# Performance work log

Measured on AMD Instinct MI355X. Metric: run time of the kernel, lower is better.

## Reference

```python
import jax, jax.numpy as jnp
import numpy as np

B, T, N, F_IN = 8, 12, 10000, 1
H = 32          # hidden_size
K = 2           # gnn_kernel (diffusion steps)
HORIZON = 12
E = 320000      # n_nodes * avg_degree 32


def setup_inputs() -> dict:
    key = jax.random.key(0)
    ks = jax.random.split(key, 12)
    s = 0.1  # weight scale to keep GRU in sane range
    return {
        "x": jax.random.normal(ks[0], (B, T, N, F_IN), jnp.float32),
        "edge_index": jax.random.randint(ks[1], (2, E), 0, N, dtype=jnp.int64),
        "edge_weight": jax.random.uniform(ks[2], (E,), jnp.float32),
        "enc_w": jax.random.normal(ks[3], (F_IN, H), jnp.float32) * s,
        "enc_b": jnp.zeros((H,), jnp.float32),
        "node_emb": jax.random.normal(ks[4], (N, H), jnp.float32) * s,
        "w_ih": jax.random.normal(ks[5], (3 * H, H), jnp.float32) * s,
        "w_hh": jax.random.normal(ks[6], (3 * H, H), jnp.float32) * s,
        "b_ih": jnp.zeros((3 * H,), jnp.float32),
        "b_hh": jnp.zeros((3 * H,), jnp.float32),
        "filt_w": jax.random.normal(ks[7], ((2 * K + 1) * H, H), jnp.float32) * s,
        "filt_b": jnp.zeros((H,), jnp.float32),
        "dec_w": jax.random.normal(ks[8], (H, F_IN * HORIZON), jnp.float32) * s,
        "dec_b": jnp.zeros((F_IN * HORIZON,), jnp.float32),
    }


def _gru_last(xs, w_ih, w_hh, b_ih, b_hh):
    # xs: [t, bn, H] -> last hidden state [bn, H]
    t, bn, h = xs.shape
    gx = jnp.einsum('tbh,gh->tbg', xs, w_ih) + b_ih  # [t, bn, 3H]

    def step(hid, gx_t):
        gh = hid @ w_hh.T + b_hh
        xr, xz, xn = jnp.split(gx_t, 3, axis=-1)
        hr, hz, hn = jnp.split(gh, 3, axis=-1)
        r = jax.nn.sigmoid(xr + hr)
        z = jax.nn.sigmoid(xz + hz)
        n_ = jnp.tanh(xn + r * hn)
        hid = (1.0 - z) * n_ + z * hid
        return hid, None

    h0 = jnp.zeros((bn, h), xs.dtype)
    h_last, _ = jax.lax.scan(step, h0, gx)
    return h_last


def _propagate(x, src, tgt, w, n):
    # x: [b, n, H]; out[:, tgt] += w * x[:, src]
    msgs = x[:, src, :] * w[None, :, None]  # [b, E, H]
    return jnp.zeros_like(x).at[:, tgt, :].add(msgs)


def reference(x, edge_index, edge_weight, enc_w, enc_b, node_emb,
              w_ih, w_hh, b_ih, b_hh, filt_w, filt_b, dec_w, dec_b):
    b, t, n, f_in = x.shape
    h = enc_w.shape[1]

    # ---- encoder + node embeddings ----
    x_enc = x @ enc_w + enc_b                       # [b, t, n, H]
    x_emb = x_enc + node_emb[None, None]            # broadcast add

    # ---- temporal GRU (per node, batch_first, last state) ----
    xs = jnp.transpose(x_emb, (1, 0, 2, 3)).reshape(t, b * n, h)
    h_time = _gru_last(xs, w_ih, w_hh, b_ih, b_hh).reshape(b, n, h)

    # ---- DiffConv: k-hop forward + backward diffusion ----
    src, tgt = edge_index[0], edge_index[1]
    deg_f = jnp.zeros((n,), edge_weight.dtype).at[tgt].add(edge_weight)
    w_f = edge_weight / jnp.where(deg_f[tgt] > 0, deg_f[tgt], 1.0)
    deg_b = jnp.zeros((n,), edge_weight.dtype).at[src].add(edge_weight)
    w_b = edge_weight / jnp.where(deg_b[src] > 0, deg_b[src], 1.0)

    outs = [h_time]  # root weight
    x_sup = h_time
    for _ in range(K):  # forward transition hops
        x_sup = _propagate(x_sup, src, tgt, w_f, n)
        outs.append(x_sup)
    x_sup = h_time
    for _ in range(K):  # backward (reversed edges) hops
        x_sup = _propagate(x_sup, tgt, src, w_b, n)
        outs.append(x_sup)
    z = jnp.concatenate(outs, axis=-1) @ filt_w + filt_b  # [b, n, H]

    # ---- decoder + rearrange 'b n (t f) -> b t n f' ----
    out = z @ dec_w + dec_b                                # [b, n, horizon*f_in]
    out = out.reshape(b, n, HORIZON, f_in)
    return jnp.transpose(out, (0, 2, 1, 3))                # [b, horizon, n, f_in]
```

## Files before the change

### kernel.cpp

```cpp
#include <hip/hip_runtime.h>
#include <hip/hip_fp16.h>

#define BB 8
#define TT 12
#define NN 10000
#define HH 32
#define EE 320000
#define HOR 12
#define NCB 157

static __device__ __forceinline__ float sigm(float x) {
    return __builtin_amdgcn_rcpf(1.0f + __expf(-x));
}
static __device__ __forceinline__ float tanh_fast(float x) {
    return 1.0f - 2.0f * __builtin_amdgcn_rcpf(1.0f + __expf(2.0f * x));
}
static __device__ __forceinline__ float2 uph2(unsigned u) {
    __half2 h = *(__half2*)&u;
    return __half22float2(h);
}
static __device__ __forceinline__ unsigned pkh2(float a, float b) {
    __half2 h = __floats2half2_rn(a, b);
    return *(unsigned*)&h;
}

typedef _Float16 f16x4 __attribute__((ext_vector_type(4)));
typedef float    f32x4 __attribute__((ext_vector_type(4)));

__global__ void k_zero(uint4* __restrict__ p, int n4) {
    int i = blockIdx.x * blockDim.x + threadIdx.x;
    if (i < n4) p[i] = (uint4){0u, 0u, 0u, 0u};
}

__global__ void k_cbhist(const float* __restrict__ node_emb, const float* __restrict__ enc_b,
                     const float* __restrict__ w_ih, const float* __restrict__ b_ih,
                     const float* __restrict__ b_hh,
                     const float* __restrict__ enc_w, const float* __restrict__ filt_w,
                     const float* __restrict__ filt_b, const float* __restrict__ dec_w,
                     const float* __restrict__ dec_b,
                     float* __restrict__ CB, float* __restrict__ A,
                     float* __restrict__ W2, float* __restrict__ b2,
                     const int* __restrict__ ei,
                     int* cnt_f, int* cnt_b) {
    __shared__ float sw[96*36];
    __shared__ float semb[64*36];
    __shared__ float sbias[96];
    int bid = blockIdx.x;
    int tid = threadIdx.x;
    if (bid < NCB) {
        int n0 = bid * 64;
        for (int i = tid; i < 96*32; i += 256) {
            int g = i >> 5, h = i & 31;
            sw[g*36 + h] = w_ih[i];
        }
        for (int i = tid; i < 64*32; i += 256) {
            int row = i >> 5, h = i & 31;
            int n = n0 + row; if (n >= NN) n = NN-1;
            semb[row*36 + h] = enc_b[h] + node_emb[(size_t)n*32 + h];
        }
        if (tid < 96) sbias[tid] = b_ih[tid] + (tid < 64 ? b_hh[tid] : 0.f);
        __syncthreads();
        #pragma unroll 1
        for (int i = 0; i < 24; i++) {
            int o = i*256 + tid;
            int row = o / 96, g = o - row*96;
            int n = n0 + row;
            if (n < NN) {
                float s = sbias[g];
                const float4* ev = (const float4*)(semb + row*36);
                const float4* wv = (const float4*)(sw + g*36);
                #pragma unroll
                for (int q = 0; q < 8; q++) {
                    float4 e = ev[q], w = wv[q];
                    s = fmaf(e.x, w.x, s); s = fmaf(e.y, w.y, s);
                    s = fmaf(e.z, w.z, s); s = fmaf(e.w, w.w, s);
                }
                CB[(size_t)n*96 + g] = s;
            }
        }
    } else if (bid == NCB) {
        for (int i = tid; i < 96 + 160*12 + 12; i += blockDim.x) {
            if (i < 96) {
                float s = 0.f;
                for (int h = 0; h < HH; h++) s += enc_w[h] * w_ih[i*HH + h];
                A[i] = s;
            } else if (i < 96 + 1920) {
                int j = i - 96; int c = j / 12, o = j % 12;
                float s = 0.f;
                for (int h = 0; h < HH; h++) s += filt_w[c*HH + h] * dec_w[h*12 + o];
                W2[j] = s;
            } else {
                int o = i - 2016;
                float s = dec_b[o];
                for (int h = 0; h < HH; h++) s += filt_b[h] * dec_w[h*12 + o];
                b2[o] = s;
            }
        }
    } else {
        int e = (bid - NCB - 1) * 256 + tid;
        int s = ei[e], t = ei[EE + e];
        atomicAdd(&cnt_f[t], 1);
        atomicAdd(&cnt_b[s], 1);
    }
}

__global__ void k_scan(const int* __restrict__ cnt_f, int* off_f, int* cur_f,
                       const int* __restrict__ cnt_b, int* off_b, int* cur_b) {
    const int* cnt; int* off; int* cur;
    if (blockIdx.x == 0) { cnt = cnt_f; off = off_f; cur = cur_f; }
    else                 { cnt = cnt_b; off = off_b; cur = cur_b; }
    __shared__ int part[1024];
    int t = threadIdx.x;
    const int CH = (NN + 1023) / 1024;
    int beg = t * CH, end = min(beg + CH, NN);
    int s = 0;
    for (int i = beg; i < end; i++) s += cnt[i];
    part[t] = s;
    __syncthreads();
    for (int d = 1; d < 1024; d <<= 1) {
        int add = (t >= d) ? part[t - d] : 0;
        __syncthreads();
        part[t] += add;
        __syncthreads();
    }
    int run = part[t] - s;
    for (int i = beg; i < end; i++) {
        off[i] = run; cur[i] = run; run += cnt[i];
    }
    if (t == 1023) off[NN] = part[1023];
}

__global__ void k_fill(const int* __restrict__ ei, const float* __restrict__ ew,
                       int* cur_f, int* csr_f_idx, float* csr_f_w,
                       int* cur_b, int* csr_b_idx, float* csr_b_w) {
    int e = blockIdx.x * blockDim.x + threadIdx.x;
    int s = ei[e], t = ei[EE + e]; float w = ew[e];
    int pf = atomicAdd(&cur_f[t], 1); csr_f_idx[pf] = s; csr_f_w[pf] = w;
    int pb = atomicAdd(&cur_b[s], 1); csr_b_idx[pb] = t; csr_b_w[pb] = w;
}

__global__ __launch_bounds__(256) void k_gru(const float* __restrict__ x,
                      const float* __restrict__ CB, const float* __restrict__ Ag,
                      const float* __restrict__ w_hh, const float* __restrict__ b_hh,
                      __half* __restrict__ hout16) {
    __shared__ unsigned sW[1536];
    __shared__ __half  shh[4][16*40];
    __shared__ float   sx[64][12];
    int tid = threadIdx.x;
    int r0b = blockIdx.x * 64;

    for (int d = tid; d < 1536; d += 256) {
        int fi = d >> 1, epair = d & 1;
        int l = fi & 63, tk = fi >> 6;
        int gt = tk >> 1, kh = tk & 1;
        int gate = 16*gt + (l & 15);
        int k = kh*16 + ((l >> 4) << 2) + 2*epair;
        sW[d] = pkh2(w_hh[gate*32 + k], w_hh[gate*32 + k + 1]);
    }
    for (int i = tid; i < 64*12; i += 256) {
        int row = i / 12, t = i - row*12;
        int r = r0b + row; int b = r / NN, n = r - b*NN;
        sx[row][t] = x[((size_t)b*TT + t)*NN + n];
    }
    __syncthreads();

    const int wv = tid >> 6, l = tid & 63;
    const int c = l & 15, m = l >> 4;
    const int r0w = r0b + wv*16;

    int bb[4], nn_[4];
    #pragma unroll
    for (int q = 0; q < 4; q++) {
        int r = r0w + 4*m + q;
        bb[q] = r / NN; nn_[q] = r - bb[q]*NN;
    }

    float cNx[2][4];
    f32x4 crv[2], czv[2], cnv[2];
    float aRj[2], aZj[2], aNj[2], bn0c[2];
    #pragma unroll
    for (int t2 = 0; t2 < 2; t2++) {
        int j = 16*t2 + c;
        #pragma unroll
        for (int q = 0; q < 4; q++) {
            const float* cb = CB + (size_t)nn_[q]*96;
            crv[t2][q] = cb[j];
            czv[t2][q] = cb[32 + j];
            cNx[t2][q] = cb[64 + j];
        }
        bn0c[t2] = b_hh[64 + j];
        cnv[t2] = (f32x4){bn0c[t2], bn0c[t2], bn0c[t2], bn0c[t2]};
        aRj[t2] = Ag[j]; aZj[t2] = Ag[32 + j]; aNj[t2] = Ag[64 + j];
    }

    f16x4 bf[12];
    #pragma unroll
    for (int i = 0; i < 12; i++) {
        unsigned long long v = *(const unsigned long long*)(sW + (i*64 + l)*2);
        bf[i] = __builtin_bit_cast(f16x4, v);
    }

    __half* hb = shh[wv];
    float own[2][4];
    {
        #pragma unroll
        for (int t2 = 0; t2 < 2; t2++)
        #pragma unroll
        for (int q = 0; q < 4; q++) {
            float xv = sx[wv*16 + 4*m + q][0];
            float rr = sigm(fmaf(xv, aRj[t2], crv[t2][q]));
            float zz = sigm(fmaf(xv, aZj[t2], czv[t2][q]));
            float nv = tanh_fast(fmaf(xv, aNj[t2], cNx[t2][q]) + rr * bn0c[t2]);
            own[t2][q] = (1.f - zz) * nv;
        }
    }
    #pragma unroll
    for (int t2 = 0; t2 < 2; t2++)
    #pragma unroll
    for (int q = 0; q < 4; q++)
        hb[(4*m + q)*40 + 16*t2 + c] = __float2half_rn(own[t2][q]);

    #pragma unroll 1
    for (int t = 1; t < TT; t++) {
        asm volatile("s_waitcnt lgkmcnt(0)" ::: "memory");
        __builtin_amdgcn_sched_barrier(0);
        unsigned long long va0 = *(const unsigned long long*)(hb + c*40 + m*4);
        unsigned long long va1 = *(const unsigned long long*)(hb + c*40 + 16 + m*4);
        f16x4 a0 = __builtin_bit_cast(f16x4, va0);
        f16x4 a1 = __builtin_bit_cast(f16x4, va1);
        float xq[4];
        #pragma unroll
        for (int q = 0; q < 4; q++) xq[q] = sx[wv*16 + 4*m + q][t];

        f32x4 aR[2], aZ[2], aN[2];
        #pragma unroll
        for (int t2 = 0; t2 < 2; t2++) {
            aR[t2] = __builtin_amdgcn_mfma_f32_16x16x16f16(a0, bf[(t2    )*2    ], crv[t2], 0, 0, 0);
            aR[t2] = __builtin_amdgcn_mfma_f32_16x16x16f16(a1, bf[(t2    )*2 + 1], aR[t2], 0, 0, 0);
            aZ[t2] = __builtin_amdgcn_mfma_f32_16x16x16f16(a0, bf[(2 + t2)*2    ], czv[t2], 0, 0, 0);
            aZ[t2] = __builtin_amdgcn_mfma_f32_16x16x16f16(a1, bf[(2 + t2)*2 + 1], aZ[t2], 0, 0, 0);
            aN[t2] = __builtin_amdgcn_mfma_f32_16x16x16f16(a0, bf[(4 + t2)*2    ], cnv[t2], 0, 0, 0);
            aN[t2] = __builtin_amdgcn_mfma_f32_16x16x16f16(a1, bf[(4 + t2)*2 + 1], aN[t2], 0, 0, 0);
        }
        #pragma unroll
        for (int t2 = 0; t2 < 2; t2++)
        #pragma unroll
        for (int q = 0; q < 4; q++) {
            float rr = sigm(fmaf(xq[q], aRj[t2], aR[t2][q]));
            float zz = sigm(fmaf(xq[q], aZj[t2], aZ[t2][q]));
            float nv = tanh_fast(fmaf(xq[q], aNj[t2], cNx[t2][q]) + rr * aN[t2][q]);
            own[t2][q] = (1.f - zz) * nv + zz * own[t2][q];
        }
        if (t < TT-1) {
            #pragma unroll
            for (int t2 = 0; t2 < 2; t2++)
            #pragma unroll
            for (int q = 0; q < 4; q++)
                hb[(4*m + q)*40 + 16*t2 + c] = __float2half_rn(own[t2][q]);
        }
    }
    #pragma unroll
    for (int t2 = 0; t2 < 2; t2++)
    #pragma unroll
    for (int q = 0; q < 4; q++)
        hout16[((size_t)nn_[q]*BB + bb[q])*HH + 16*t2 + c] = __float2half(own[t2][q]);
}

__global__ __launch_bounds__(256) void k_prop(
        const __half* __restrict__ xF, const __half* __restrict__ xB,
        __half* __restrict__ yF16, __half* __restrict__ yB16,
        const int* __restrict__ offF, const int* __restrict__ idxF, const float* __restrict__ wF,
        const int* __restrict__ offB, const int* __restrict__ idxB, const float* __restrict__ wB) {
    int wid = threadIdx.x >> 6;
    int l   = threadIdx.x & 63;
    int nd = blockIdx.x * 4 + wid;
    int n = nd >> 1, dir = nd & 1;
    const unsigned* xu = (const unsigned*)(dir ? xB : xF);
    const int* off = dir ? offB : offF;
    const int* idx = dir ? idxB : idxF;
    const float* w = dir ? wB : wF;

    int e0 = off[n], e1 = off[n+1];
    float a0 = 0.f, a1 = 0.f, a2 = 0.f, a3 = 0.f, ws = 0.f;
    int e = e0;
    for (; e + 8 <= e1; e += 8) {
        int   s0 = idx[e],   s1 = idx[e+1], s2 = idx[e+2], s3 = idx[e+3];
        int   s4 = idx[e+4], s5 = idx[e+5], s6 = idx[e+6], s7 = idx[e+7];
        float w0 = w[e],     w1 = w[e+1],   w2 = w[e+2],   w3 = w[e+3];
        float w4 = w[e+4],   w5 = w[e+5],   w6 = w[e+6],   w7 = w[e+7];
        uint2 u0 = *(const uint2*)(xu + ((size_t)s0 << 7) + 2*l);
        uint2 u1 = *(const uint2*)(xu + ((size_t)s1 << 7) + 2*l);
        uint2 u2 = *(const uint2*)(xu + ((size_t)s2 << 7) + 2*l);
        uint2 u3 = *(const uint2*)(xu + ((size_t)s3 << 7) + 2*l);
        uint2 u4 = *(const uint2*)(xu + ((size_t)s4 << 7) + 2*l);
        uint2 u5 = *(const uint2*)(xu + ((size_t)s5 << 7) + 2*l);
        uint2 u6 = *(const uint2*)(xu + ((size_t)s6 << 7) + 2*l);
        uint2 u7 = *(const uint2*)(xu + ((size_t)s7 << 7) + 2*l);
        ws += ((w0 + w1) + (w2 + w3)) + ((w4 + w5) + (w6 + w7));
        float2 f;
        f = uph2(u0.x); a0 = fmaf(w0, f.x, a0); a1 = fmaf(w0, f.y, a1);
        f = uph2(u0.y); a2 = fmaf(w0, f.x, a2); a3 = fmaf(w0, f.y, a3);
        f = uph2(u1.x); a0 = fmaf(w1, f.x, a0); a1 = fmaf(w1, f.y, a1);
        f = uph2(u1.y); a2 = fmaf(w1, f.x, a2); a3 = fmaf(w1, f.y, a3);
        f = uph2(u2.x); a0 = fmaf(w2, f.x, a0); a1 = fmaf(w2, f.y, a1);
        f = uph2(u2.y); a2 = fmaf(w2, f.x, a2); a3 = fmaf(w2, f.y, a3);
        f = uph2(u3.x); a0 = fmaf(w3, f.x, a0); a1 = fmaf(w3, f.y, a1);
        f = uph2(u3.y); a2 = fmaf(w3, f.x, a2); a3 = fmaf(w3, f.y, a3);
        f = uph2(u4.x); a0 = fmaf(w4, f.x, a0); a1 = fmaf(w4, f.y, a1);
        f = uph2(u4.y); a2 = fmaf(w4, f.x, a2); a3 = fmaf(w4, f.y, a3);
        f = uph2(u5.x); a0 = fmaf(w5, f.x, a0); a1 = fmaf(w5, f.y, a1);
        f = uph2(u5.y); a2 = fmaf(w5, f.x, a2); a3 = fmaf(w5, f.y, a3);
        f = uph2(u6.x); a0 = fmaf(w6, f.x, a0); a1 = fmaf(w6, f.y, a1);
        f = uph2(u6.y); a2 = fmaf(w6, f.x, a2); a3 = fmaf(w6, f.y, a3);
        f = uph2(u7.x); a0 = fmaf(w7, f.x, a0); a1 = fmaf(w7, f.y, a1);
        f = uph2(u7.y); a2 = fmaf(w7, f.x, a2); a3 = fmaf(w7, f.y, a3);
    }
    for (; e < e1; ++e) {
        int s0 = idx[e]; float w0 = w[e];
        uint2 u0 = *(const uint2*)(xu + ((size_t)s0 << 7) + 2*l);
        ws += w0;
        float2 f;
        f = uph2(u0.x); a0 = fmaf(w0, f.x, a0); a1 = fmaf(w0, f.y, a1);
        f = uph2(u0.y); a2 = fmaf(w0, f.x, a2); a3 = fmaf(w0, f.y, a3);
    }
    float inv = ws > 0.f ? __builtin_amdgcn_rcpf(ws) : 1.0f;
    a0 *= inv; a1 *= inv; a2 *= inv; a3 *= inv;
    unsigned* yh = (unsigned*)(dir ? yB16 : yF16);
    uint2 oh; oh.x = pkh2(a0, a1); oh.y = pkh2(a2, a3);
    *(uint2*)(yh + ((size_t)n << 7) + 2*l) = oh;
}

__global__ __launch_bounds__(256) void k_dec(const __half* __restrict__ p0,
                     const __half* __restrict__ p1, const __half* __restrict__ p2,
                     const __half* __restrict__ p3, const __half* __restrict__ p4,
                     const float* __restrict__ W2, const float* __restrict__ b2,
                     float* __restrict__ out) {
    __shared__ float sW[1920];
    __shared__ float sb[12];
    __shared__ float part[128][13];
    int tid = threadIdx.x;
    for (int i = tid; i < 1920; i += 256) sW[i] = W2[i];
    if (tid < 12) sb[tid] = b2[tid];
    __syncthreads();
    int lr = tid & 127, half = tid >> 7;
    int r = blockIdx.x * 128 + lr;
    int b = r / NN, n = r - b*NN;
    size_t base = ((size_t)n * BB + b) * HH;
    float a[12];
    if (half == 0) {
        uint4 v[12];
        {
            const uint4* q0 = (const uint4*)(p0 + base);
            const uint4* q1 = (const uint4*)(p1 + base);
            const uint4* q2 = (const uint4*)(p2 + base);
            #pragma unroll
            for (int q = 0; q < 4; q++) { v[q] = q0[q]; v[4+q] = q1[q]; v[8+q] = q2[q]; }
        }
        #pragma unroll
        for (int o = 0; o < 12; o++) a[o] = sb[o];
        #pragma unroll
        for (int pi = 0; pi < 3; pi++)
        #pragma unroll
        for (int q = 0; q < 4; q++) {
            uint4 vv = v[pi*4 + q];
            float2 f0 = uph2(vv.x), f1 = uph2(vv.y), f2 = uph2(vv.z), f3 = uph2(vv.w);
            float pv[8] = {f0.x, f0.y, f1.x, f1.y, f2.x, f2.y, f3.x, f3.y};
            #pragma unroll
            for (int k = 0; k < 8; k++) {
                const float* wrow = sW + (pi*32 + q*8 + k) * 12;
                #pragma unroll
                for (int o = 0; o < 12; o++) a[o] = fmaf(pv[k], wrow[o], a[o]);
            }
        }
    } else {
        uint4 v[8];
        {
            const uint4* q3 = (const uint4*)(p3 + base);
            const uint4* q4 = (const uint4*)(p4 + base);
            #pragma unroll
            for (int q = 0; q < 4; q++) { v[q] = q3[q]; v[4+q] = q4[q]; }
        }
        #pragma unroll
        for (int o = 0; o < 12; o++) a[o] = 0.f;
        #pragma unroll
        for (int pi = 0; pi < 2; pi++)
        #pragma unroll
        for (int q = 0; q < 4; q++) {
            uint4 vv = v[pi*4 + q];
            float2 f0 = uph2(vv.x), f1 = uph2(vv.y), f2 = uph2(vv.z), f3 = uph2(vv.w);
            float pv[8] = {f0.x, f0.y, f1.x, f1.y, f2.x, f2.y, f3.x, f3.y};
            #pragma unroll
            for (int k = 0; k < 8; k++) {
                const float* wrow = sW + ((pi+3)*32 + q*8 + k) * 12;
                #pragma unroll
                for (int o = 0; o < 12; o++) a[o] = fmaf(pv[k], wrow[o], a[o]);
            }
        }
        #pragma unroll
        for (int o = 0; o < 12; o++) part[lr][o] = a[o];
    }
    __syncthreads();
    if (half == 0) {
        #pragma unroll
        for (int t = 0; t < HOR; t++)
            out[((size_t)(b*HOR + t))*NN + n] = a[t] + part[lr][t];
    }
}

extern "C" void kernel_launch(void* const* d_in, const int* in_sizes, int n_in,
                              void* d_out, int out_size, void* d_ws, size_t ws_size,
                              hipStream_t stream) {
    const float* x      = (const float*)d_in[0];
    const int*   ei     = (const int*)d_in[1];
    const float* ew     = (const float*)d_in[2];
    const float* enc_w  = (const float*)d_in[3];
    const float* enc_b  = (const float*)d_in[4];
    const float* nemb   = (const float*)d_in[5];
    const float* w_ih   = (const float*)d_in[6];
    const float* w_hh   = (const float*)d_in[7];
    const float* b_ih   = (const float*)d_in[8];
    const float* b_hh   = (const float*)d_in[9];
    const float* filt_w = (const float*)d_in[10];
    const float* filt_b = (const float*)d_in[11];
    const float* dec_w  = (const float*)d_in[12];
    const float* dec_b  = (const float*)d_in[13];
    float* out = (float*)d_out;

    char* p = (char*)d_ws;
    auto alloc = [&](size_t bytes) -> char* {
        char* q = p; p += (bytes + 255) & ~(size_t)255; return q;
    };
    char* zero_base = p;
    int*   cnt_f = (int*)  alloc((size_t)NN*4);
    int*   cnt_b = (int*)  alloc((size_t)NN*4);
    size_t zero_bytes = (size_t)(p - zero_base);
    int zero_n4 = (int)(zero_bytes / 16);

    const size_t SROW = (size_t)BB*NN*HH;
    __half* h16    = (__half*)alloc(SROW*2);
    __half* a16    = (__half*)alloc(SROW*2);
    __half* b16    = (__half*)alloc(SROW*2);
    __half* c16    = (__half*)alloc(SROW*2);
    __half* d16    = (__half*)alloc(SROW*2);
    float* CB     = (float*)alloc((size_t)NN*96*4);
    float* A      = (float*)alloc(96*4);
    float* W2     = (float*)alloc(1920*4);
    float* b2     = (float*)alloc(12*4);
    int*   off_f  = (int*)  alloc((size_t)(NN+1)*4);
    int*   off_b  = (int*)  alloc((size_t)(NN+1)*4);
    int*   cur_f  = (int*)  alloc((size_t)NN*4);
    int*   cur_b  = (int*)  alloc((size_t)NN*4);
    int*   cfi    = (int*)  alloc((size_t)EE*4);
    float* cfw    = (float*)alloc((size_t)EE*4);
    int*   cbi    = (int*)  alloc((size_t)EE*4);
    float* cbw    = (float*)alloc((size_t)EE*4);

    k_zero<<<(zero_n4 + 255)/256, 256, 0, stream>>>((uint4*)zero_base, zero_n4);

    k_cbhist<<<NCB + 1 + EE/256, 256, 0, stream>>>(nemb, enc_b, w_ih, b_ih, b_hh,
                                       enc_w, filt_w, filt_b, dec_w, dec_b,
                                       CB, A, W2, b2, ei, cnt_f, cnt_b);
    k_scan<<<2, 1024, 0, stream>>>(cnt_f, off_f, cur_f, cnt_b, off_b, cur_b);
    k_fill<<<EE/256, 256, 0, stream>>>(ei, ew, cur_f, cfi, cfw, cur_b, cbi, cbw);

    k_gru<<<1250, 256, 0, stream>>>(x, CB, A, w_hh, b_hh, h16);

    k_prop<<<5000, 256, 0, stream>>>(h16, h16, a16, c16,
                                     off_f, cfi, cfw, off_b, cbi, cbw);
    k_prop<<<5000, 256, 0, stream>>>(a16, c16, b16, d16,
                                     off_f, cfi, cfw, off_b, cbi, cbw);

    k_dec<<<625, 256, 0, stream>>>(h16, a16, b16, c16, d16, W2, b2, out);
}
```

Measured before the change: 222.3 us.

## Fuse CSR fill into GRU launch, interleave edge data, fuse second hop with decoder

The CSR fill kernel is merged into the GRU launch as extra blocks, so edge scattering can overlap with the recurrent compute. Edge index and weight are packed into one uint2 array, so each gather reads a single 8-byte record. The second diffusion hop is fused with the decoder: hop-2 results stay in shared memory and feed the output projection directly, which removes two intermediate fp16 buffers and a separate decoder launch. In exchange, the decoder phase now runs on only 64 of 256 threads per block, and the GRU blocks may lose occupancy from sharing the grid with fill blocks.

```diff
diff --git a/kernel.cpp b/kernel.cpp
--- a/kernel.cpp
+++ b/kernel.cpp
@@ -130,23 +130,27 @@
     if (t == 1023) off[NN] = part[1023];
 }
 
-__global__ void k_fill(const int* __restrict__ ei, const float* __restrict__ ew,
-                       int* cur_f, int* csr_f_idx, float* csr_f_w,
-                       int* cur_b, int* csr_b_idx, float* csr_b_w) {
-    int e = blockIdx.x * blockDim.x + threadIdx.x;
-    int s = ei[e], t = ei[EE + e]; float w = ew[e];
-    int pf = atomicAdd(&cur_f[t], 1); csr_f_idx[pf] = s; csr_f_w[pf] = w;
-    int pb = atomicAdd(&cur_b[s], 1); csr_b_idx[pb] = t; csr_b_w[pb] = w;
-}
-
-__global__ __launch_bounds__(256) void k_gru(const float* __restrict__ x,
+__global__ __launch_bounds__(256) void k_grufill(const float* __restrict__ x,
                       const float* __restrict__ CB, const float* __restrict__ Ag,
                       const float* __restrict__ w_hh, const float* __restrict__ b_hh,
-                      __half* __restrict__ hout16) {
+                      __half* __restrict__ hout16,
+                      const int* __restrict__ ei, const float* __restrict__ ew,
+                      int* cur_f, uint2* __restrict__ cfe,
+                      int* cur_b, uint2* __restrict__ cbe) {
+    int tid = threadIdx.x;
+    if (blockIdx.x >= 1250) {
+        int e = (blockIdx.x - 1250) * 256 + tid;
+        int s = ei[e], t = ei[EE + e]; float w = ew[e];
+        unsigned wb = __float_as_uint(w);
+        int pf = atomicAdd(&cur_f[t], 1);
+        uint2 vf; vf.x = (unsigned)s; vf.y = wb; cfe[pf] = vf;
+        int pb = atomicAdd(&cur_b[s], 1);
+        uint2 vb; vb.x = (unsigned)t; vb.y = wb; cbe[pb] = vb;
+        return;
+    }
     __shared__ unsigned sW[1536];
     __shared__ __half  shh[4][16*40];
     __shared__ float   sx[64][12];
-    int tid = threadIdx.x;
     int r0b = blockIdx.x * 64;
 
     for (int d = tid; d < 1536; d += 256) {
@@ -266,36 +270,27 @@
         hout16[((size_t)nn_[q]*BB + bb[q])*HH + 16*t2 + c] = __float2half(own[t2][q]);
 }
 
-__global__ __launch_bounds__(256) void k_prop(
-        const __half* __restrict__ xF, const __half* __restrict__ xB,
-        __half* __restrict__ yF16, __half* __restrict__ yB16,
-        const int* __restrict__ offF, const int* __restrict__ idxF, const float* __restrict__ wF,
-        const int* __restrict__ offB, const int* __restrict__ idxB, const float* __restrict__ wB) {
-    int wid = threadIdx.x >> 6;
-    int l   = threadIdx.x & 63;
-    int nd = blockIdx.x * 4 + wid;
-    int n = nd >> 1, dir = nd & 1;
-    const unsigned* xu = (const unsigned*)(dir ? xB : xF);
-    const int* off = dir ? offB : offF;
-    const int* idx = dir ? idxB : idxF;
-    const float* w = dir ? wB : wF;
-
-    int e0 = off[n], e1 = off[n+1];
-    float a0 = 0.f, a1 = 0.f, a2 = 0.f, a3 = 0.f, ws = 0.f;
+static __device__ __forceinline__ void gather_node(
+        const unsigned* __restrict__ xu, const uint2* __restrict__ ef,
+        int e0, int e1, int l, float& a0, float& a1, float& a2, float& a3) {
+    float ws = 0.f;
+    a0 = a1 = a2 = a3 = 0.f;
     int e = e0;
     for (; e + 8 <= e1; e += 8) {
-        int   s0 = idx[e],   s1 = idx[e+1], s2 = idx[e+2], s3 = idx[e+3];
-        int   s4 = idx[e+4], s5 = idx[e+5], s6 = idx[e+6], s7 = idx[e+7];
-        float w0 = w[e],     w1 = w[e+1],   w2 = w[e+2],   w3 = w[e+3];
-        float w4 = w[e+4],   w5 = w[e+5],   w6 = w[e+6],   w7 = w[e+7];
-        uint2 u0 = *(const uint2*)(xu + ((size_t)s0 << 7) + 2*l);
-        uint2 u1 = *(const uint2*)(xu + ((size_t)s1 << 7) + 2*l);
-        uint2 u2 = *(const uint2*)(xu + ((size_t)s2 << 7) + 2*l);
-        uint2 u3 = *(const uint2*)(xu + ((size_t)s3 << 7) + 2*l);
-        uint2 u4 = *(const uint2*)(xu + ((size_t)s4 << 7) + 2*l);
-        uint2 u5 = *(const uint2*)(xu + ((size_t)s5 << 7) + 2*l);
-        uint2 u6 = *(const uint2*)(xu + ((size_t)s6 << 7) + 2*l);
-        uint2 u7 = *(const uint2*)(xu + ((size_t)s7 << 7) + 2*l);
+        uint2 q0 = ef[e],   q1 = ef[e+1], q2 = ef[e+2], q3 = ef[e+3];
+        uint2 q4 = ef[e+4], q5 = ef[e+5], q6 = ef[e+6], q7 = ef[e+7];
+        float w0 = __uint_as_float(q0.y), w1 = __uint_as_float(q1.y);
+        float w2 = __uint_as_float(q2.y), w3 = __uint_as_float(q3.y);
+        float w4 = __uint_as_float(q4.y), w5 = __uint_as_float(q5.y);
+        float w6 = __uint_as_float(q6.y), w7 = __uint_as_float(q7.y);
+        uint2 u0 = *(const uint2*)(xu + ((size_t)q0.x << 7) + 2*l);
+        uint2 u1 = *(const uint2*)(xu + ((size_t)q1.x << 7) + 2*l);
+        uint2 u2 = *(const uint2*)(xu + ((size_t)q2.x << 7) + 2*l);
+        uint2 u3 = *(const uint2*)(xu + ((size_t)q3.x << 7) + 2*l);
+        uint2 u4 = *(const uint2*)(xu + ((size_t)q4.x << 7) + 2*l);
+        uint2 u5 = *(const uint2*)(xu + ((size_t)q5.x << 7) + 2*l);
+        uint2 u6 = *(const uint2*)(xu + ((size_t)q6.x << 7) + 2*l);
+        uint2 u7 = *(const uint2*)(xu + ((size_t)q7.x << 7) + 2*l);
         ws += ((w0 + w1) + (w2 + w3)) + ((w4 + w5) + (w6 + w7));
         float2 f;
         f = uph2(u0.x); a0 = fmaf(w0, f.x, a0); a1 = fmaf(w0, f.y, a1);
@@ -316,8 +311,9 @@
         f = uph2(u7.y); a2 = fmaf(w7, f.x, a2); a3 = fmaf(w7, f.y, a3);
     }
     for (; e < e1; ++e) {
-        int s0 = idx[e]; float w0 = w[e];
-        uint2 u0 = *(const uint2*)(xu + ((size_t)s0 << 7) + 2*l);
+        uint2 q0 = ef[e];
+        float w0 = __uint_as_float(q0.y);
+        uint2 u0 = *(const uint2*)(xu + ((size_t)q0.x << 7) + 2*l);
         ws += w0;
         float2 f;
         f = uph2(u0.x); a0 = fmaf(w0, f.x, a0); a1 = fmaf(w0, f.y, a1);
@@ -325,85 +321,103 @@
     }
     float inv = ws > 0.f ? __builtin_amdgcn_rcpf(ws) : 1.0f;
     a0 *= inv; a1 *= inv; a2 *= inv; a3 *= inv;
+}
+
+__global__ __launch_bounds__(256) void k_prop(
+        const __half* __restrict__ xF, const __half* __restrict__ xB,
+        __half* __restrict__ yF16, __half* __restrict__ yB16,
+        const int* __restrict__ offF, const uint2* __restrict__ efF,
+        const int* __restrict__ offB, const uint2* __restrict__ efB) {
+    int wid = threadIdx.x >> 6;
+    int l   = threadIdx.x & 63;
+    int nd = blockIdx.x * 4 + wid;
+    int n = nd >> 1, dir = nd & 1;
+    const unsigned* xu = (const unsigned*)(dir ? xB : xF);
+    const int* off = dir ? offB : offF;
+    const uint2* ef = dir ? efB : efF;
+    float a0, a1, a2, a3;
+    gather_node(xu, ef, off[n], off[n+1], l, a0, a1, a2, a3);
     unsigned* yh = (unsigned*)(dir ? yB16 : yF16);
     uint2 oh; oh.x = pkh2(a0, a1); oh.y = pkh2(a2, a3);
     *(uint2*)(yh + ((size_t)n << 7) + 2*l) = oh;
 }
 
-__global__ __launch_bounds__(256) void k_dec(const __half* __restrict__ p0,
-                     const __half* __restrict__ p1, const __half* __restrict__ p2,
-                     const __half* __restrict__ p3, const __half* __restrict__ p4,
-                     const float* __restrict__ W2, const float* __restrict__ b2,
-                     float* __restrict__ out) {
+__global__ __launch_bounds__(256) void k_prop2dec(
+        const __half* __restrict__ aF, const __half* __restrict__ cBk,
+        const __half* __restrict__ h16,
+        const int* __restrict__ offF, const uint2* __restrict__ efF,
+        const int* __restrict__ offB, const uint2* __restrict__ efB,
+        const float* __restrict__ W2, const float* __restrict__ b2,
+        float* __restrict__ out) {
     __shared__ float sW[1920];
     __shared__ float sb[12];
-    __shared__ float part[128][13];
+    __shared__ unsigned spc[4][2][128];
     int tid = threadIdx.x;
     for (int i = tid; i < 1920; i += 256) sW[i] = W2[i];
     if (tid < 12) sb[tid] = b2[tid];
+    int wv = tid >> 6, l = tid & 63;
+    int n = blockIdx.x * 4 + wv;
+    {
+        float a0, a1, a2, a3;
+        gather_node((const unsigned*)aF, efF, offF[n], offF[n+1], l, a0, a1, a2, a3);
+        spc[wv][0][2*l]   = pkh2(a0, a1);
+        spc[wv][0][2*l+1] = pkh2(a2, a3);
+    }
+    {
+        float a0, a1, a2, a3;
+        gather_node((const unsigned*)cBk, efB, offB[n], offB[n+1], l, a0, a1, a2, a3);
+        spc[wv][1][2*l]   = pkh2(a0, a1);
+        spc[wv][1][2*l+1] = pkh2(a2, a3);
+    }
     __syncthreads();
-    int lr = tid & 127, half = tid >> 7;
-    int r = blockIdx.x * 128 + lr;
-    int b = r / NN, n = r - b*NN;
-    size_t base = ((size_t)n * BB + b) * HH;
-    float a[12];
-    if (half == 0) {
-        uint4 v[12];
-        {
-            const uint4* q0 = (const uint4*)(p0 + base);
-            const uint4* q1 = (const uint4*)(p1 + base);
-            const uint4* q2 = (const uint4*)(p2 + base);
+    if (tid < 64) {
+        int nl = tid >> 4;
+        int b  = (tid >> 1) & 7;
+        int th = tid & 1;
+        int node = blockIdx.x * 4 + nl;
+        size_t base = ((size_t)node * BB + b) * HH;
+        float a[6];
+        #pragma unroll
+        for (int o = 0; o < 6; o++) a[o] = sb[6*th + o];
+        const __half* gp[3] = {h16, aF, cBk};
+        const int wo[3] = {0, 32, 96};
+        #pragma unroll
+        for (int gi = 0; gi < 3; gi++) {
+            const uint4* pp = (const uint4*)(gp[gi] + base);
+            const float* wbase = sW + wo[gi]*12 + 6*th;
             #pragma unroll
-            for (int q = 0; q < 4; q++) { v[q] = q0[q]; v[4+q] = q1[q]; v[8+q] = q2[q]; }
-        }
-        #pragma unroll
-        for (int o = 0; o < 12; o++) a[o] = sb[o];
-        #pragma unroll
-        for (int pi = 0; pi < 3; pi++)
-        #pragma unroll
-        for (int q = 0; q < 4; q++) {
-            uint4 vv = v[pi*4 + q];
-            float2 f0 = uph2(vv.x), f1 = uph2(vv.y), f2 = uph2(vv.z), f3 = uph2(vv.w);
-            float pv[8] = {f0.x, f0.y, f1.x, f1.y, f2.x, f2.y, f3.x, f3.y};
+            for (int q = 0; q < 4; q++) {
+                uint4 v = pp[q];
+                float2 f0 = uph2(v.x), f1 = uph2(v.y), f2 = uph2(v.z), f3 = uph2(v.w);
+                float pv[8] = {f0.x, f0.y, f1.x, f1.y, f2.x, f2.y, f3.x, f3.y};
+                #pragma unroll
+                for (int k = 0; k < 8; k++) {
+                    const float* wrow = wbase + (q*8 + k)*12;
+                    #pragma unroll
+                    for (int o = 0; o < 6; o++) a[o] = fmaf(pv[k], wrow[o], a[o]);
+                }
+            }
+        }
+        #pragma unroll
+        for (int dir = 0; dir < 2; dir++) {
+            const uint4* pp = (const uint4*)&spc[nl][dir][b*16];
+            const float* wbase = sW + (64 + dir*64)*12 + 6*th;
             #pragma unroll
-            for (int k = 0; k < 8; k++) {
-                const float* wrow = sW + (pi*32 + q*8 + k) * 12;
+            for (int q = 0; q < 4; q++) {
+                uint4 v = pp[q];
+                float2 f0 = uph2(v.x), f1 = uph2(v.y), f2 = uph2(v.z), f3 = uph2(v.w);
+                float pv[8] = {f0.x, f0.y, f1.x, f1.y, f2.x, f2.y, f3.x, f3.y};
                 #pragma unroll
-                for (int o = 0; o < 12; o++) a[o] = fmaf(pv[k], wrow[o], a[o]);
+                for (int k = 0; k < 8; k++) {
+                    const float* wrow = wbase + (q*8 + k)*12;
+                    #pragma unroll
+                    for (int o = 0; o < 6; o++) a[o] = fmaf(pv[k], wrow[o], a[o]);
+                }
             }
         }
-    } else {
-        uint4 v[8];
-        {
-            const uint4* q3 = (const uint4*)(p3 + base);
-            const uint4* q4 = (const uint4*)(p4 + base);
-            #pragma unroll
-            for (int q = 0; q < 4; q++) { v[q] = q3[q]; v[4+q] = q4[q]; }
-        }
-        #pragma unroll
-        for (int o = 0; o < 12; o++) a[o] = 0.f;
-        #pragma unroll
-        for (int pi = 0; pi < 2; pi++)
-        #pragma unroll
-        for (int q = 0; q < 4; q++) {
-            uint4 vv = v[pi*4 + q];
-            float2 f0 = uph2(vv.x), f1 = uph2(vv.y), f2 = uph2(vv.z), f3 = uph2(vv.w);
-            float pv[8] = {f0.x, f0.y, f1.x, f1.y, f2.x, f2.y, f3.x, f3.y};
-            #pragma unroll
-            for (int k = 0; k < 8; k++) {
-                const float* wrow = sW + ((pi+3)*32 + q*8 + k) * 12;
-                #pragma unroll
-                for (int o = 0; o < 12; o++) a[o] = fmaf(pv[k], wrow[o], a[o]);
-            }
-        }
-        #pragma unroll
-        for (int o = 0; o < 12; o++) part[lr][o] = a[o];
-    }
-    __syncthreads();
-    if (half == 0) {
-        #pragma unroll
-        for (int t = 0; t < HOR; t++)
-            out[((size_t)(b*HOR + t))*NN + n] = a[t] + part[lr][t];
+        #pragma unroll
+        for (int o = 0; o < 6; o++)
+            out[((size_t)(b*HOR + 6*th + o))*NN + node] = a[o];
     }
 }
 
@@ -439,9 +453,7 @@
     const size_t SROW = (size_t)BB*NN*HH;
     __half* h16    = (__half*)alloc(SROW*2);
     __half* a16    = (__half*)alloc(SROW*2);
-    __half* b16    = (__half*)alloc(SROW*2);
     __half* c16    = (__half*)alloc(SROW*2);
-    __half* d16    = (__half*)alloc(SROW*2);
     float* CB     = (float*)alloc((size_t)NN*96*4);
     float* A      = (float*)alloc(96*4);
     float* W2     = (float*)alloc(1920*4);
@@ -450,10 +462,8 @@
     int*   off_b  = (int*)  alloc((size_t)(NN+1)*4);
     int*   cur_f  = (int*)  alloc((size_t)NN*4);
     int*   cur_b  = (int*)  alloc((size_t)NN*4);
-    int*   cfi    = (int*)  alloc((size_t)EE*4);
-    float* cfw    = (float*)alloc((size_t)EE*4);
-    int*   cbi    = (int*)  alloc((size_t)EE*4);
-    float* cbw    = (float*)alloc((size_t)EE*4);
+    uint2* cfe    = (uint2*)alloc((size_t)EE*8);
+    uint2* cbe    = (uint2*)alloc((size_t)EE*8);
 
     k_zero<<<(zero_n4 + 255)/256, 256, 0, stream>>>((uint4*)zero_base, zero_n4);
 
@@ -461,14 +471,13 @@
                                        enc_w, filt_w, filt_b, dec_w, dec_b,
                                        CB, A, W2, b2, ei, cnt_f, cnt_b);
     k_scan<<<2, 1024, 0, stream>>>(cnt_f, off_f, cur_f, cnt_b, off_b, cur_b);
-    k_fill<<<EE/256, 256, 0, stream>>>(ei, ew, cur_f, cfi, cfw, cur_b, cbi, cbw);
-
-    k_gru<<<1250, 256, 0, stream>>>(x, CB, A, w_hh, b_hh, h16);
+
+    k_grufill<<<2500, 256, 0, stream>>>(x, CB, A, w_hh, b_hh, h16,
+                                        ei, ew, cur_f, cfe, cur_b, cbe);
 
     k_prop<<<5000, 256, 0, stream>>>(h16, h16, a16, c16,
-                                     off_f, cfi, cfw, off_b, cbi, cbw);
-    k_prop<<<5000, 256, 0, stream>>>(a16, c16, b16, d16,
-                                     off_f, cfi, cfw, off_b, cbi, cbw);
-
-    k_dec<<<625, 256, 0, stream>>>(h16, a16, b16, c16, d16, W2, b2, out);
-}
+                                     off_f, cfe, off_b, cbe);
+    k_prop2dec<<<2500, 256, 0, stream>>>(a16, c16, h16,
+                                         off_f, cfe, off_b, cbe,
+                                         W2, b2, out);
+}
```

Measured after the change: 201.7 us. 1.1x faster.
